# Optimization experiments

Hardware: AMD Instinct MI355X
Metric: run time of the kernel (lower is better)

Reference implementation:

```python
import jax, jax.numpy as jnp
import numpy as np

NUM_BLOCKS = 4   # opt['num_blocks']
BK = 64          # base_num_kernels
GC = 16          # growth_channel = BK/4
NC = 3           # num_channels
K = 3            # kernel_size
HK = 1           # half kernel
B_RES = 0.2      # opt['B'] residual scaling
N_DB = NUM_BLOCKS * 3  # dense blocks total (3 per RRDB)

# dense-block conv in/out channels (positions 1..5)
_DB_IO = [(BK, GC), (BK + GC, GC), (BK + 2 * GC, GC), (BK + 3 * GC, GC), (BK + 4 * GC, BK)]


def setup_inputs() -> dict:
    key = jax.random.key(0)
    ks = iter(jax.random.split(key, 32))

    def nrm(shape, scale=0.05):
        return jax.random.normal(next(ks), shape, dtype=jnp.float32) * scale

    inp = {}
    inp["x"] = jax.random.normal(next(ks), (1, NC, 96, 96), dtype=jnp.float32)
    inp["c1_w"] = nrm((BK, NC, K, K)); inp["c1_b"] = nrm((BK,))
    for i, (ic, oc) in enumerate(_DB_IO):
        inp[f"db_w{i+1}"] = nrm((N_DB, oc, ic, K, K))
        inp[f"db_b{i+1}"] = nrm((N_DB, oc))
    inp["c2_w"] = nrm((BK, BK, K, K)); inp["c2_b"] = nrm((BK,))
    inp["fc1_w"] = nrm((3, 256)); inp["fc1_b"] = nrm((256,))
    inp["fc2_w"] = nrm((256, BK * NC * K * K)); inp["fc2_b"] = nrm((BK * NC * K * K,))
    inp["scale_factor"] = 2
    return inp


def _lrelu(t):
    return jnp.where(t > 0, t, 0.2 * t)


def _conv(h, w, b):
    y = jax.lax.conv_general_dilated(h, w, (1, 1), [(HK, HK), (HK, HK)],
                                     dimension_numbers=('NCHW', 'OIHW', 'NCHW'))
    return y + b[None, :, None, None]


def reference(x, c1_w, c1_b, db_w1, db_b1, db_w2, db_b2, db_w3, db_b3,
              db_w4, db_b4, db_w5, db_b5, c2_w, c2_b,
              fc1_w, fc1_b, fc2_w, fc2_b, scale_factor):
    sf = int(scale_factor)

    def dense_block(h, d):
        c1 = _lrelu(_conv(h, db_w1[d], db_b1[d]))
        c2 = _lrelu(_conv(jnp.concatenate([h, c1], 1), db_w2[d], db_b2[d]))
        c3 = _lrelu(_conv(jnp.concatenate([h, c1, c2], 1), db_w3[d], db_b3[d]))
        c4 = _lrelu(_conv(jnp.concatenate([h, c1, c2, c3], 1), db_w4[d], db_b4[d]))
        return _conv(jnp.concatenate([h, c1, c2, c3, c4], 1), db_w5[d], db_b5[d])

    x0 = _conv(x, c1_w, c1_b)
    feat = x0
    for blk in range(NUM_BLOCKS):  # RRDB chain
        base = blk * 3
        d1 = dense_block(feat, base) * B_RES + feat
        d2 = dense_block(d1, base + 1) * B_RES + d1
        d3 = dense_block(d2, base + 2) * B_RES + d2
        feat = d3 * B_RES + feat
    feat = x0 + _conv(feat, c2_w, c2_b)

    Bb, _, H, W = x.shape
    oH, oW = H * sf, W * sf
    # coordinate features exactly as in torch code (column-wise tiling)
    x_col = jnp.tile(jnp.arange(oH, dtype=x.dtype), oW)
    y_col = jnp.tile(jnp.arange(oW, dtype=x.dtype), oH)
    sf_col = jnp.full((oH * oW,), float(sf), dtype=x.dtype)
    winp = jnp.stack([x_col, y_col, sf_col], axis=1)  # [oH*oW, 3]
    h1 = _lrelu(winp @ fc1_w + fc1_b)
    # per-output-pixel dynamic filters: [B, C, oH, oW, BK, K, K]
    wts = (h1 @ fc2_w + fc2_b).reshape(Bb, NC, oH, oW, BK, K, K)

    # zero-padded sliding 3x3 patches of features: [B, BK, H, W, K, K]
    fpad = jnp.pad(feat, ((0, 0), (0, 0), (HK, HK), (HK, HK)))
    patches = jnp.stack([jnp.stack([fpad[:, :, di:di + H, dj:dj + W]
                                    for dj in range(K)], axis=-1)
                         for di in range(K)], axis=-2)
    ip = jnp.arange(oH) // sf  # i_prime per output row
    jp = jnp.arange(oW) // sf  # j_prime per output col
    pu = patches[:, :, ip][:, :, :, jp]  # [B, BK, oH, oW, K, K]

    # fused gather-multiply-reduce (the original per-pixel loop)
    out = jnp.einsum('bchwkij,bkhwij->bchw', wts, pu)
    return out
```

## Files before the change

### kernel.cpp

```cpp
#include <hip/hip_runtime.h>

#define Hh 96
#define Ww 96
#define HW 9216
#define NPIX 589824

typedef __attribute__((ext_vector_type(8))) short bf16x8;
typedef __attribute__((ext_vector_type(4))) float f32x4;

__device__ __forceinline__ unsigned short f2bf(float f) {
    unsigned int u = __float_as_uint(f);
    u += 0x7fff + ((u >> 16) & 1);
    return (unsigned short)(u >> 16);
}

__global__ __launch_bounds__(256) void prep_w_k(
    const float* __restrict__ w0, const float* __restrict__ w1,
    const float* __restrict__ w2, const float* __restrict__ w3,
    const float* __restrict__ w4, const float* __restrict__ c2w,
    unsigned short* __restrict__ wb)
{
    int idx = blockIdx.x * 256 + threadIdx.x;
    const int DSEG = 152064, TOT = 12 * 152064;
    if (idx >= TOT + 36864) return;
    float val;
    if (idx < TOT) {
        int d = idx / DSEG, rem = idx - d * DSEG;
        if (rem < 59904) {
            int e, L, IC; const float* wp;
            if      (rem < 10368) { e = rem;         L = 72;  IC = 64;  wp = w0; }
            else if (rem < 25344) { e = rem - 10368; L = 104; IC = 80;  wp = w1; }
            else if (rem < 40320) { e = rem - 25344; L = 104; IC = 96;  wp = w2; }
            else                  { e = rem - 40320; L = 136; IC = 112; wp = w3; }
            int row = e / L, col = e - row * L;
            int tap = row / 16, oc = row - tap * 16;
            val = (col < IC) ? wp[(((size_t)d * 16 + oc) * IC + col) * 9 + tap] : 0.f;
        } else {
            int e = rem - 59904;
            int kq = e / 23040, r = e - kq * 23040;
            int row = r / 40, col = r - row * 40;
            int tap = row / 64, oc = row - tap * 64;
            val = (col < 32)
                ? w4[(((size_t)d * 64 + oc) * 128 + kq * 32 + col) * 9 + tap] : 0.f;
        }
    } else {
        int e = idx - TOT;
        int tap = e / 4096, r = e & 4095;
        int oc = r >> 6, icp = r & 63;
        val = c2w[((size_t)(oc * 64 + icp)) * 9 + tap];
    }
    wb[idx] = f2bf(val);
}

__global__ __launch_bounds__(256) void c1_k(
    const float* __restrict__ x, const float* __restrict__ w,
    const float* __restrict__ bias,
    float* __restrict__ x0f, unsigned short* __restrict__ dba)
{
    __shared__ float sw[1728];
    __shared__ float sb[64];
    int tid = threadIdx.x;
    for (int i = tid; i < 1728; i += 256) sw[i] = w[i];
    if (tid < 64) sb[tid] = bias[tid];
    __syncthreads();
    int px = blockIdx.x * 256 + tid;
    int gy = px / 96, gx = px - (px / 96) * 96;
    float in[3][3][3];
    #pragma unroll
    for (int c = 0; c < 3; ++c)
        #pragma unroll
        for (int dy = 0; dy < 3; ++dy)
            #pragma unroll
            for (int dx = 0; dx < 3; ++dx) {
                int yy = gy - 1 + dy, xx = gx - 1 + dx;
                in[c][dy][dx] = (yy >= 0 && yy < 96 && xx >= 0 && xx < 96)
                                ? x[c * HW + yy * 96 + xx] : 0.f;
            }
    for (int oc = 0; oc < 64; ++oc) {
        float acc = sb[oc];
        const float* wp = &sw[oc * 27];
        #pragma unroll
        for (int c = 0; c < 3; ++c)
            #pragma unroll
            for (int dy = 0; dy < 3; ++dy)
                #pragma unroll
                for (int dx = 0; dx < 3; ++dx)
                    acc += wp[(c * 3 + dy) * 3 + dx] * in[c][dy][dx];
        x0f[(size_t)px * 64 + oc] = acc;
        dba[(size_t)px * 64 + oc] = f2bf(acc);
    }
}

#define CSTR 136
#define RSTR 16
#define ACTHW 34816
#define SLOTHW 23040

__device__ __forceinline__ void gll_copy(const unsigned short* __restrict__ g,
                                         unsigned short* l, int nhw, int tid)
{
    for (int off = tid * 8; off < nhw; off += 2048)
        __builtin_amdgcn_global_load_lds(
            (const __attribute__((address_space(1))) void*)(g + off),
            (__attribute__((address_space(3))) void*)(l + off), 16, 0, 0);
}

template<int NS, int BS, int ICP, int ICPP, int OCH>
__device__ __forceinline__ void growth_stage(
    unsigned short* s, const unsigned short* wl,
    const float* __restrict__ bias, int wid, int l16, int q)
{
    constexpr int NPXr = NS * NS;
    constexpr int NT = (NPXr + 15) / 16;
    constexpr int MX = (NT + 3) / 4;
    f32x4 acc[MX];
    int lp0[MX], outp[MX];
    bool ok[MX];
    #pragma unroll
    for (int i = 0; i < MX; ++i) {
        int nt = wid + i * 4;
        int p  = nt * 16 + l16;
        bool live = (nt < NT) && (p < NPXr);
        ok[i] = live;
        int pc = live ? p : 0;
        int r = pc / NS, c = pc - (pc / NS) * NS;
        lp0[i]  = (BS - 1 + r) * RSTR + (BS - 1 + c);
        outp[i] = (BS + r) * RSTR + (BS + c);
        acc[i]  = (f32x4){0.f, 0.f, 0.f, 0.f};
    }
    for (int kb = 0; kb < ICP; kb += 32) {
        #pragma unroll
        for (int tap = 0; tap < 9; ++tap) {
            const int dy = tap / 3, dx = tap - dy * 3;
            bf16x8 a = *(const bf16x8*)&wl[(tap * 16 + l16) * ICPP + kb + q * 8];
            #pragma unroll
            for (int i = 0; i < MX; ++i) {
                bf16x8 b = *(const bf16x8*)&s[(lp0[i] + dy * RSTR + dx) * CSTR + kb + q * 8];
                acc[i] = __builtin_amdgcn_mfma_f32_16x16x32_bf16(a, b, acc[i], 0, 0, 0);
            }
        }
    }
    const float4 bv = *(const float4*)&bias[q * 4];
    #pragma unroll
    for (int i = 0; i < MX; ++i) {
        if (!ok[i]) continue;
        float v0 = acc[i][0] + bv.x; v0 = v0 > 0.f ? v0 : 0.2f * v0;
        float v1 = acc[i][1] + bv.y; v1 = v1 > 0.f ? v1 : 0.2f * v1;
        float v2 = acc[i][2] + bv.z; v2 = v2 > 0.f ? v2 : 0.2f * v2;
        float v3 = acc[i][3] + bv.w; v3 = v3 > 0.f ? v3 : 0.2f * v3;
        ushort4 o = {f2bf(v0), f2bf(v1), f2bf(v2), f2bf(v3)};
        *(ushort4*)&s[outp[i] * CSTR + OCH + q * 4] = o;
    }
}

template<int KQ>
__device__ __forceinline__ void cv5_quarter(
    const unsigned short* s, const unsigned short* wl,
    int mt, int l16, int q, const int* lp0c, f32x4* acc)
{
    #pragma unroll
    for (int tap = 0; tap < 9; ++tap) {
        const int dy = tap / 3, dx = tap - dy * 3;
        bf16x8 a = *(const bf16x8*)&wl[(tap * 64 + mt * 16 + l16) * 40 + q * 8];
        #pragma unroll
        for (int nt = 0; nt < 3; ++nt) {
            bf16x8 b = *(const bf16x8*)&s[(lp0c[nt] + dy * RSTR + dx) * CSTR + KQ * 32 + q * 8];
            acc[nt] = __builtin_amdgcn_mfma_f32_16x16x32_bf16(a, b, acc[nt], 0, 0, 0);
        }
    }
}

__global__ __launch_bounds__(256) void dense_block_k(
    const unsigned short* __restrict__ hin,
    const unsigned short* __restrict__ wb,
    const float* __restrict__ b1, const float* __restrict__ b2,
    const float* __restrict__ b3, const float* __restrict__ b4,
    const float* __restrict__ b5,
    float alpha, const float* __restrict__ r1, float beta,
    const float* __restrict__ r2, float gamma,
    unsigned short* __restrict__ hout,
    float* out_fp)
{
    const int tile = blockIdx.x;
    const int tx0 = (tile & 15) * 6, ty0 = (tile >> 4) * 6;
    const int tid = threadIdx.x;
    const int wid = tid >> 6, lane = tid & 63;
    const int l16 = lane & 15, q = lane >> 4;

    __shared__ unsigned short s[ACTHW + 2 * SLOTHW];
    unsigned short* sA = s + ACTHW;
    unsigned short* sB = s + ACTHW + SLOTHW;

    gll_copy(wb, sA, 10368, tid);

    for (int i = tid; i < 256 * 16; i += 256) {
        int p = i >> 4, g = i & 15;
        int ly = p >> 4, lx = p & 15;
        int gy = ty0 - 5 + ly, gx = tx0 - 5 + lx;
        uint4 v = {0u, 0u, 0u, 0u};
        if (g < 8 && gy >= 0 && gy < 96 && gx >= 0 && gx < 96)
            v = *(const uint4*)&hin[(size_t)(gy * 96 + gx) * 64 + g * 8];
        *(uint4*)&s[p * CSTR + g * 8] = v;
    }
    __syncthreads();

    gll_copy(wb + 10368, sB, 14976, tid);
    growth_stage<14, 1,  64,  72,  64>(s, sA, b1, wid, l16, q);
    __syncthreads();

    gll_copy(wb + 25344, sA, 14976, tid);
    growth_stage<12, 2,  96, 104,  80>(s, sB, b2, wid, l16, q);
    __syncthreads();

    gll_copy(wb + 40320, sB, 19584, tid);
    growth_stage<10, 3,  96, 104,  96>(s, sA, b3, wid, l16, q);
    __syncthreads();

    gll_copy(wb + 59904, sA, 23040, tid);
    growth_stage< 8, 4, 128, 136, 112>(s, sB, b4, wid, l16, q);
    __syncthreads();

    {
        const int mt = wid;
        int lp0c[3];
        bool okc[3];
        int rowc[3], colc[3];
        #pragma unroll
        for (int nt = 0; nt < 3; ++nt) {
            int p = nt * 16 + l16;
            okc[nt] = (p < 36);
            int pc = okc[nt] ? p : 0;
            rowc[nt] = pc / 6; colc[nt] = pc - (pc / 6) * 6;
            lp0c[nt] = (4 + rowc[nt]) * RSTR + (4 + colc[nt]);
        }
        f32x4 acc[3];
        acc[0] = (f32x4){0.f,0.f,0.f,0.f};
        acc[1] = (f32x4){0.f,0.f,0.f,0.f};
        acc[2] = (f32x4){0.f,0.f,0.f,0.f};

        gll_copy(wb + 59904 + 23040, sB, 23040, tid);
        cv5_quarter<0>(s, sA, mt, l16, q, lp0c, acc);
        __syncthreads();

        gll_copy(wb + 59904 + 2 * 23040, sA, 23040, tid);
        cv5_quarter<1>(s, sB, mt, l16, q, lp0c, acc);
        __syncthreads();

        gll_copy(wb + 59904 + 3 * 23040, sB, 23040, tid);
        cv5_quarter<2>(s, sA, mt, l16, q, lp0c, acc);
        __syncthreads();

        cv5_quarter<3>(s, sB, mt, l16, q, lp0c, acc);

        const float4 bv = *(const float4*)&b5[mt * 16 + q * 4];
        const int ocb = mt * 16 + q * 4;
        #pragma unroll
        for (int nt = 0; nt < 3; ++nt) {
            if (!okc[nt]) continue;
            size_t pix = (size_t)((ty0 + rowc[nt]) * 96 + tx0 + colc[nt]);
            float4 res1, res2;
            if (r1) res1 = *(const float4*)&r1[pix * 64 + ocb];
            if (r2) res2 = *(const float4*)&r2[pix * 64 + ocb];
            float vv[4];
            #pragma unroll
            for (int r = 0; r < 4; ++r) {
                float v = acc[nt][r] + ((const float*)&bv)[r];
                v *= alpha;
                if (r1) v += beta  * ((const float*)&res1)[r];
                if (r2) v += gamma * ((const float*)&res2)[r];
                vv[r] = v;
            }
            ushort4 o = {f2bf(vv[0]), f2bf(vv[1]), f2bf(vv[2]), f2bf(vv[3])};
            *(ushort4*)&hout[pix * 64 + ocb] = o;
            float4 of = {vv[0], vv[1], vv[2], vv[3]};
            *(float4*)&out_fp[pix * 64 + ocb] = of;
        }
    }
}

__global__ __launch_bounds__(256) void conv_mfma_k(
    const unsigned short* __restrict__ act, int cstride, int IC, int ICp,
    const unsigned short* __restrict__ wb,
    const float* __restrict__ bias,
    float alpha, const float* __restrict__ r1, float beta,
    float* __restrict__ out_fp)
{
    const int tile = blockIdx.x;
    const int tx0 = (tile % 12) * 8, ty0 = (tile / 12) * 4;
    const int tid = threadIdx.x;
    const int wid = tid >> 6, lane = tid & 63;
    const int l16 = lane & 15, q = lane >> 4;
    const int stride = ICp + 8;

    __shared__ unsigned short s[60 * 136];

    const int NG = ICp >> 3;
    for (int i = tid; i < 60 * NG; i += 256) {
        int hp = i / NG, g = i - hp * NG;
        int row = hp / 10, col = hp - row * 10;
        int gy = ty0 - 1 + row, gx = tx0 - 1 + col;
        int gc = g * 8;
        uint4 v = {0u, 0u, 0u, 0u};
        if (gy >= 0 && gy < 96 && gx >= 0 && gx < 96 && gc < IC)
            v = *reinterpret_cast<const uint4*>(
                    &act[(size_t)(gy * 96 + gx) * cstride + gc]);
        *reinterpret_cast<uint4*>(&s[hp * stride + gc]) = v;
    }
    __syncthreads();

    const int mt = wid;
    f32x4 acc0 = {0.f, 0.f, 0.f, 0.f}, acc1 = {0.f, 0.f, 0.f, 0.f};
    const int arow = (mt * 16 + l16) * ICp + q * 8;
    const int yy0 = l16 >> 3, xx0 = l16 & 7;
    const int yy1 = 2 + (l16 >> 3), xx1 = l16 & 7;
    for (int icb = 0; icb < ICp; icb += 32) {
        #pragma unroll
        for (int tap = 0; tap < 9; ++tap) {
            const int dy = tap / 3, dx = tap - dy * 3;
            bf16x8 a = *(const bf16x8*)&wb[(size_t)tap * 64 * ICp + arow + icb];
            bf16x8 b0 = *(const bf16x8*)&s[((yy0 + dy) * 10 + xx0 + dx) * stride + icb + q * 8];
            acc0 = __builtin_amdgcn_mfma_f32_16x16x32_bf16(a, b0, acc0, 0, 0, 0);
            bf16x8 b1 = *(const bf16x8*)&s[((yy1 + dy) * 10 + xx1 + dx) * stride + icb + q * 8];
            acc1 = __builtin_amdgcn_mfma_f32_16x16x32_bf16(a, b1, acc1, 0, 0, 0);
        }
    }
    const float4 bv = *(const float4*)&bias[mt * 16 + q * 4];
    #pragma unroll
    for (int nt = 0; nt < 2; ++nt) {
        f32x4 acc = nt ? acc1 : acc0;
        int p = nt * 16 + l16;
        size_t pix = (size_t)((ty0 + (p >> 3)) * 96 + tx0 + (p & 7));
        int ocb = mt * 16 + q * 4;
        float4 res1;
        if (r1) res1 = *(const float4*)&r1[pix * 64 + ocb];
        float4 o;
        #pragma unroll
        for (int r = 0; r < 4; ++r) {
            float v = acc[r] + ((const float*)&bv)[r];
            v *= alpha;
            if (r1) v += beta * ((const float*)&res1)[r];
            ((float*)&o)[r] = v;
        }
        *(float4*)&out_fp[pix * 64 + ocb] = o;
    }
}

__global__ __launch_bounds__(256) void mlp_k(
    const float* __restrict__ fc1_w, const float* __restrict__ fc1_b,
    const float* __restrict__ fc2_w, const float* __restrict__ fc2_b,
    float* __restrict__ WtT)
{
    const int f0 = blockIdx.x * 64, t0 = blockIdx.y * 64;
    const int tid = threadIdx.x;
    const int ft = tid & 15, tt = tid >> 4;
    __shared__ float sa[256], sc[256];
    __shared__ float swt[64][64];
    sa[tid] = fc1_w[tid] + fc1_w[256 + tid];
    sc[tid] = 2.f * fc1_w[512 + tid] + fc1_b[tid];
    float acc[4][4] = {};
    const float tbase = (float)(t0 + tt * 4);
    for (int jc = 0; jc < 256; jc += 64) {
        __syncthreads();
        for (int i = tid; i < 4096; i += 256) {
            int j = i >> 6, f = i & 63;
            swt[j][f] = fc2_w[(size_t)(jc + j) * 1728 + f0 + f];
        }
        __syncthreads();
        for (int j = 0; j < 64; ++j) {
            float4 wv = *(const float4*)&swt[j][ft * 4];
            float aj = sa[jc + j], cj = sc[jc + j];
            #pragma unroll
            for (int v = 0; v < 4; ++v) {
                float h = aj * (tbase + (float)v) + cj;
                h = (h > 0.f) ? h : 0.2f * h;
                acc[0][v] += h * wv.x;
                acc[1][v] += h * wv.y;
                acc[2][v] += h * wv.z;
                acc[3][v] += h * wv.w;
            }
        }
    }
    #pragma unroll
    for (int u = 0; u < 4; ++u) {
        int f = f0 + ft * 4 + u;
        float b = fc2_b[f];
        float4 o = {acc[u][0] + b, acc[u][1] + b, acc[u][2] + b, acc[u][3] + b};
        *(float4*)&WtT[(size_t)f * 192 + t0 + tt * 4] = o;
    }
}

__global__ __launch_bounds__(256) void dynfilter_k(
    const float* __restrict__ feat,
    const float* __restrict__ WtT,
    float* __restrict__ out)
{
    const int h   = blockIdx.y;
    const int w0  = blockIdx.x * 64;
    const int tid = threadIdx.x;
    const int lw  = tid & 63, kc = tid >> 6;
    const int ybase = h / 2 - 1;
    const int x0lo  = w0 / 2 - 1;

    __shared__ float s_f[64][3][36];
    __shared__ float s_red[4][64];

    for (int i = tid; i < 64 * 102; i += 256) {
        int k = i & 63, j = i >> 6;
        int di = j / 34, col = j - di * 34;
        int yv = ybase + di, xv = x0lo + col;
        float v = 0.f;
        if (yv >= 0 && yv < Hh && xv >= 0 && xv < Ww)
            v = feat[(size_t)(yv * Ww + xv) * 64 + k];
        s_f[k][di][col] = v;
    }
    __syncthreads();

    const int w = w0 + lw;
    const int qq = w % 3;
    const int t = (h % 3) * 64 + w / 3;
    const int lx = (w / 2 - 1) - x0lo;
    const float* Wp = WtT + (size_t)(qq * 576 + kc * 144) * 192 + t;
    float acc = 0.f;
    for (int k = 0; k < 16; ++k) {
        #pragma unroll
        for (int di = 0; di < 3; ++di)
            #pragma unroll
            for (int dj = 0; dj < 3; ++dj)
                acc += s_f[kc * 16 + k][di][lx + dj]
                     * Wp[(size_t)(k * 9 + di * 3 + dj) * 192];
    }
    s_red[kc][lw] = acc;
    __syncthreads();
    if (kc == 0) {
        float v = s_red[0][lw] + s_red[1][lw] + s_red[2][lw] + s_red[3][lw];
        int o = h * 192 + w;
        out[o] = v;
        out[36864 + o] = v;
        out[2 * 36864 + o] = v;
    }
}

extern "C" void kernel_launch(void* const* d_in, const int* in_sizes, int n_in,
                              void* d_out, int out_size, void* d_ws, size_t ws_size,
                              hipStream_t stream)
{
    const float* x     = (const float*)d_in[0];
    const float* c1_w  = (const float*)d_in[1];
    const float* c1_b  = (const float*)d_in[2];
    const float* dbw[5] = {(const float*)d_in[3], (const float*)d_in[5],
                           (const float*)d_in[7], (const float*)d_in[9],
                           (const float*)d_in[11]};
    const float* dbb[5] = {(const float*)d_in[4], (const float*)d_in[6],
                           (const float*)d_in[8], (const float*)d_in[10],
                           (const float*)d_in[12]};
    const float* c2_w  = (const float*)d_in[13];
    const float* c2_b  = (const float*)d_in[14];
    const float* fc1_w = (const float*)d_in[15];
    const float* fc1_b = (const float*)d_in[16];
    const float* fc2_w = (const float*)d_in[17];
    const float* fc2_b = (const float*)d_in[18];

    float* ws    = (float*)d_ws;
    float* x0f   = ws;
    float* hfA   = ws + (size_t)NPIX;
    float* hfB   = ws + 2 * (size_t)NPIX;
    float* featf = ws + 3 * (size_t)NPIX;
    unsigned short* dbaA = (unsigned short*)(ws + 4 * (size_t)NPIX);
    unsigned short* dbaB = dbaA + (size_t)9216 * 64;
    unsigned short* wb   = dbaB + (size_t)9216 * 64;
    float* WtT = (float*)(wb + (size_t)1861632 + 128);
    float* ff  = hfA;

    prep_w_k<<<7272, 256, 0, stream>>>(dbw[0], dbw[1], dbw[2], dbw[3], dbw[4],
                                       c2_w, wb);
    c1_k<<<36, 256, 0, stream>>>(x, c1_w, c1_b, x0f, dbaA);

    for (int d = 0; d < 12; ++d) {
        unsigned short* hin  = (d & 1) ? dbaB : dbaA;
        unsigned short* hout = (d & 1) ? dbaA : dbaB;
        const float* featprev = (d < 3) ? x0f : featf;
        const unsigned short* wseg = wb + (size_t)d * 152064;
        const float* b1 = dbb[0] + (size_t)d * 16;
        const float* b2 = dbb[1] + (size_t)d * 16;
        const float* b3 = dbb[2] + (size_t)d * 16;
        const float* b4 = dbb[3] + (size_t)d * 16;
        const float* b5 = dbb[4] + (size_t)d * 64;
        int pos = d % 3;
        if (pos == 0)
            dense_block_k<<<256, 256, 0, stream>>>(hin, wseg, b1, b2, b3, b4, b5,
                0.2f, featprev, 1.f, nullptr, 0.f, hout, hfA);
        else if (pos == 1)
            dense_block_k<<<256, 256, 0, stream>>>(hin, wseg, b1, b2, b3, b4, b5,
                0.2f, hfA, 1.f, nullptr, 0.f, hout, hfB);
        else
            dense_block_k<<<256, 256, 0, stream>>>(hin, wseg, b1, b2, b3, b4, b5,
                0.04f, hfB, 0.2f, featprev, 1.f, hout, featf);
    }

    conv_mfma_k<<<288, 256, 0, stream>>>(dbaA, 64, 64, 64,
        wb + (size_t)12 * 152064, c2_b, 1.f, x0f, 1.f, ff);

    mlp_k<<<dim3(27, 3), 256, 0, stream>>>(fc1_w, fc1_b, fc2_w, fc2_b, WtT);
    dynfilter_k<<<dim3(3, 192), 256, 0, stream>>>(ff, WtT, (float*)d_out);
}
```

Measured before the change: 344.4 us.

## Rewrite final conv as 6x6-tile MFMA kernel with weights staged in LDS

The generic final 3x3 conv kernel (8x4 tiles, 288 blocks, weights read from global memory) is replaced by a specialised kernel using 6x6 output tiles over 256 blocks. Weights are repacked into two 32-channel halves with padded rows and copied into shared memory with an asynchronous global-to-LDS copy, the second half overlapping the first half's MFMAs. The goal is one wave of blocks matching the CU count and fewer global weight loads. In exchange, 12 of the 48 MFMA columns are wasted on padding and the kernel is hard-coded to 64 channels.

```diff
diff --git a/kernel.cpp b/kernel.cpp
--- a/kernel.cpp
+++ b/kernel.cpp
@@ -22,7 +22,7 @@
 {
     int idx = blockIdx.x * 256 + threadIdx.x;
     const int DSEG = 152064, TOT = 12 * 152064;
-    if (idx >= TOT + 36864) return;
+    if (idx >= TOT + 46080) return;
     float val;
     if (idx < TOT) {
         int d = idx / DSEG, rem = idx - d * DSEG;
@@ -45,9 +45,11 @@
         }
     } else {
         int e = idx - TOT;
-        int tap = e / 4096, r = e & 4095;
-        int oc = r >> 6, icp = r & 63;
-        val = c2w[((size_t)(oc * 64 + icp)) * 9 + tap];
+        int kh = e / 23040, r = e - kh * 23040;
+        int row = r / 40, col = r - row * 40;
+        int tap = row / 64, oc = row - tap * 64;
+        val = (col < 32)
+            ? c2w[((size_t)(oc * 64) + kh * 32 + col) * 9 + tap] : 0.f;
     }
     wb[idx] = f2bf(val);
 }
@@ -278,69 +280,90 @@
     }
 }
 
-__global__ __launch_bounds__(256) void conv_mfma_k(
-    const unsigned short* __restrict__ act, int cstride, int IC, int ICp,
-    const unsigned short* __restrict__ wb,
+__global__ __launch_bounds__(256) void c2_mfma6_k(
+    const unsigned short* __restrict__ act,
+    const unsigned short* __restrict__ wb2,
     const float* __restrict__ bias,
-    float alpha, const float* __restrict__ r1, float beta,
+    const float* __restrict__ r1,
     float* __restrict__ out_fp)
 {
     const int tile = blockIdx.x;
-    const int tx0 = (tile % 12) * 8, ty0 = (tile / 12) * 4;
+    const int tx0 = (tile & 15) * 6, ty0 = (tile >> 4) * 6;
     const int tid = threadIdx.x;
     const int wid = tid >> 6, lane = tid & 63;
     const int l16 = lane & 15, q = lane >> 4;
-    const int stride = ICp + 8;
-
-    __shared__ unsigned short s[60 * 136];
-
-    const int NG = ICp >> 3;
-    for (int i = tid; i < 60 * NG; i += 256) {
-        int hp = i / NG, g = i - hp * NG;
-        int row = hp / 10, col = hp - row * 10;
-        int gy = ty0 - 1 + row, gx = tx0 - 1 + col;
-        int gc = g * 8;
+    const int mt  = wid;
+
+    __shared__ unsigned short s[64 * 72 + 2 * SLOTHW];
+    unsigned short* sA = s + 64 * 72;
+    unsigned short* sB = sA + SLOTHW;
+
+    gll_copy(wb2, sA, 23040, tid);
+
+    for (int i = tid; i < 64 * 8; i += 256) {
+        int p = i >> 3, g = i & 7;
+        int ly = p >> 3, lx = p & 7;
+        int gy = ty0 - 1 + ly, gx = tx0 - 1 + lx;
         uint4 v = {0u, 0u, 0u, 0u};
-        if (gy >= 0 && gy < 96 && gx >= 0 && gx < 96 && gc < IC)
-            v = *reinterpret_cast<const uint4*>(
-                    &act[(size_t)(gy * 96 + gx) * cstride + gc]);
-        *reinterpret_cast<uint4*>(&s[hp * stride + gc]) = v;
-    }
-    __syncthreads();
-
-    const int mt = wid;
-    f32x4 acc0 = {0.f, 0.f, 0.f, 0.f}, acc1 = {0.f, 0.f, 0.f, 0.f};
-    const int arow = (mt * 16 + l16) * ICp + q * 8;
-    const int yy0 = l16 >> 3, xx0 = l16 & 7;
-    const int yy1 = 2 + (l16 >> 3), xx1 = l16 & 7;
-    for (int icb = 0; icb < ICp; icb += 32) {
-        #pragma unroll
-        for (int tap = 0; tap < 9; ++tap) {
-            const int dy = tap / 3, dx = tap - dy * 3;
-            bf16x8 a = *(const bf16x8*)&wb[(size_t)tap * 64 * ICp + arow + icb];
-            bf16x8 b0 = *(const bf16x8*)&s[((yy0 + dy) * 10 + xx0 + dx) * stride + icb + q * 8];
-            acc0 = __builtin_amdgcn_mfma_f32_16x16x32_bf16(a, b0, acc0, 0, 0, 0);
-            bf16x8 b1 = *(const bf16x8*)&s[((yy1 + dy) * 10 + xx1 + dx) * stride + icb + q * 8];
-            acc1 = __builtin_amdgcn_mfma_f32_16x16x32_bf16(a, b1, acc1, 0, 0, 0);
-        }
-    }
+        if (gy >= 0 && gy < 96 && gx >= 0 && gx < 96)
+            v = *(const uint4*)&act[(size_t)(gy * 96 + gx) * 64 + g * 8];
+        *(uint4*)&s[p * 72 + g * 8] = v;
+    }
+    __syncthreads();
+
+    gll_copy(wb2 + SLOTHW, sB, 23040, tid);
+
+    int lp0c[3];
+    bool okc[3];
+    int rowc[3], colc[3];
+    #pragma unroll
+    for (int nt = 0; nt < 3; ++nt) {
+        int p = nt * 16 + l16;
+        okc[nt] = (p < 36);
+        int pc = okc[nt] ? p : 0;
+        rowc[nt] = pc / 6; colc[nt] = pc - (pc / 6) * 6;
+        lp0c[nt] = rowc[nt] * 8 + colc[nt];
+    }
+    f32x4 acc[3];
+    acc[0] = (f32x4){0.f,0.f,0.f,0.f};
+    acc[1] = (f32x4){0.f,0.f,0.f,0.f};
+    acc[2] = (f32x4){0.f,0.f,0.f,0.f};
+
+    #pragma unroll
+    for (int tap = 0; tap < 9; ++tap) {
+        const int dy = tap / 3, dx = tap - dy * 3;
+        bf16x8 a = *(const bf16x8*)&sA[(tap * 64 + mt * 16 + l16) * 40 + q * 8];
+        #pragma unroll
+        for (int nt = 0; nt < 3; ++nt) {
+            bf16x8 b = *(const bf16x8*)&s[(lp0c[nt] + dy * 8 + dx) * 72 + q * 8];
+            acc[nt] = __builtin_amdgcn_mfma_f32_16x16x32_bf16(a, b, acc[nt], 0, 0, 0);
+        }
+    }
+    __syncthreads();
+
+    #pragma unroll
+    for (int tap = 0; tap < 9; ++tap) {
+        const int dy = tap / 3, dx = tap - dy * 3;
+        bf16x8 a = *(const bf16x8*)&sB[(tap * 64 + mt * 16 + l16) * 40 + q * 8];
+        #pragma unroll
+        for (int nt = 0; nt < 3; ++nt) {
+            bf16x8 b = *(const bf16x8*)&s[(lp0c[nt] + dy * 8 + dx) * 72 + 32 + q * 8];
+            acc[nt] = __builtin_amdgcn_mfma_f32_16x16x32_bf16(a, b, acc[nt], 0, 0, 0);
+        }
+    }
+
     const float4 bv = *(const float4*)&bias[mt * 16 + q * 4];
-    #pragma unroll
-    for (int nt = 0; nt < 2; ++nt) {
-        f32x4 acc = nt ? acc1 : acc0;
-        int p = nt * 16 + l16;
-        size_t pix = (size_t)((ty0 + (p >> 3)) * 96 + tx0 + (p & 7));
-        int ocb = mt * 16 + q * 4;
-        float4 res1;
-        if (r1) res1 = *(const float4*)&r1[pix * 64 + ocb];
+    const int ocb = mt * 16 + q * 4;
+    #pragma unroll
+    for (int nt = 0; nt < 3; ++nt) {
+        if (!okc[nt]) continue;
+        size_t pix = (size_t)((ty0 + rowc[nt]) * 96 + tx0 + colc[nt]);
+        float4 res1 = *(const float4*)&r1[pix * 64 + ocb];
         float4 o;
         #pragma unroll
-        for (int r = 0; r < 4; ++r) {
-            float v = acc[r] + ((const float*)&bv)[r];
-            v *= alpha;
-            if (r1) v += beta * ((const float*)&res1)[r];
-            ((float*)&o)[r] = v;
-        }
+        for (int r = 0; r < 4; ++r)
+            ((float*)&o)[r] = acc[nt][r] + ((const float*)&bv)[r]
+                              + ((const float*)&res1)[r];
         *(float4*)&out_fp[pix * 64 + ocb] = o;
     }
 }
@@ -468,10 +491,10 @@
     unsigned short* dbaA = (unsigned short*)(ws + 4 * (size_t)NPIX);
     unsigned short* dbaB = dbaA + (size_t)9216 * 64;
     unsigned short* wb   = dbaB + (size_t)9216 * 64;
-    float* WtT = (float*)(wb + (size_t)1861632 + 128);
+    float* WtT = (float*)(wb + (size_t)1870848 + 128);
     float* ff  = hfA;
 
-    prep_w_k<<<7272, 256, 0, stream>>>(dbw[0], dbw[1], dbw[2], dbw[3], dbw[4],
+    prep_w_k<<<7308, 256, 0, stream>>>(dbw[0], dbw[1], dbw[2], dbw[3], dbw[4],
                                        c2_w, wb);
     c1_k<<<36, 256, 0, stream>>>(x, c1_w, c1_b, x0f, dbaA);
 
@@ -497,8 +520,8 @@
                 0.04f, hfB, 0.2f, featprev, 1.f, hout, featf);
     }
 
-    conv_mfma_k<<<288, 256, 0, stream>>>(dbaA, 64, 64, 64,
-        wb + (size_t)12 * 152064, c2_b, 1.f, x0f, 1.f, ff);
+    c2_mfma6_k<<<256, 256, 0, stream>>>(dbaA, wb + (size_t)12 * 152064,
+                                        c2_b, x0f, ff);
 
     mlp_k<<<dim3(27, 3), 256, 0, stream>>>(fc1_w, fc1_b, fc2_w, fc2_b, WtT);
     dynfilter_k<<<dim3(3, 192), 256, 0, stream>>>(ff, WtT, (float*)d_out);
```

Measured after the change: 341.0 us (median of 2 runs). About the same (-1.0%).
